# Optimization experiments

Hardware: AMD Instinct MI355X
Metric: run time of the kernel (lower is better)

The kernel has to match this reference:

```python
import jax, jax.numpy as jnp
import numpy as np

N_QUBITS = 10
DEPTH = 6


def _ry(theta):
    # RY(theta) = [[cos(t/2), -sin(t/2)], [sin(t/2), cos(t/2)]]
    c = jnp.cos(theta / 2)
    s = jnp.sin(theta / 2)
    return jnp.stack([jnp.stack([c, -s]), jnp.stack([s, c])]).astype(jnp.complex64)


def _rot(phi, theta, omega):
    # PennyLane Rot(phi, theta, omega) = RZ(omega) RY(theta) RZ(phi)
    c = jnp.cos(theta / 2)
    s = jnp.sin(theta / 2)
    ep = jnp.exp(-0.5j * (phi + omega).astype(jnp.complex64))
    em = jnp.exp(-0.5j * (phi - omega).astype(jnp.complex64))
    return jnp.stack([
        jnp.stack([ep * c, -jnp.conj(em) * s]),
        jnp.stack([em * s, jnp.conj(ep) * c]),
    ])


def _apply_1q(psi, U, w):
    # psi: (2,)*n statevector; apply 2x2 unitary U on qubit axis w
    psi = jnp.tensordot(U, psi, axes=([1], [w]))
    return jnp.moveaxis(psi, 0, w)


def _apply_cnot(psi, c, t):
    # flip target axis t on the control=1 slice of axis c
    psi = jnp.moveaxis(psi, (c, t), (0, 1))
    psi = jnp.concatenate([psi[:1], psi[1:, ::-1]], axis=0)
    return jnp.moveaxis(psi, (0, 1), (c, t))


def _circuit(angles, weights):
    """RY encoding + StronglyEntanglingLayers + PauliZ expvals. angles: (n,), weights: (depth, n, 3)."""
    n = N_QUBITS
    psi = jnp.zeros((2,) * n, jnp.complex64).at[(0,) * n].set(1.0)
    for i in range(n):
        psi = _apply_1q(psi, _ry(angles[i]), i)
    for l in range(DEPTH):
        for i in range(n):
            psi = _apply_1q(psi, _rot(weights[l, i, 0], weights[l, i, 1], weights[l, i, 2]), i)
        r = (l % (n - 1)) + 1  # default StronglyEntanglingLayers range schedule
        for i in range(n):
            psi = _apply_cnot(psi, i, (i + r) % n)
    p = psi.real ** 2 + psi.imag ** 2  # probabilities, shape (2,)*n
    exps = []
    for i in range(n):
        pm = jnp.moveaxis(p, i, 0).reshape(2, -1).sum(axis=1)
        exps.append(pm[0] - pm[1])  # <Z_i>
    return jnp.stack(exps)


def setup_inputs() -> dict:
    key = jax.random.key(0)
    ks = jax.random.split(key, 5)
    B, F, C = 8192, 1024, 10
    x = jax.random.normal(ks[0], (B, F), jnp.float32)
    W_proj = jax.random.normal(ks[1], (N_QUBITS, F), jnp.float32) / np.sqrt(F).astype(np.float32)
    weights = 0.01 * jax.random.normal(ks[2], (DEPTH, N_QUBITS, 3), jnp.float32)
    W_out = jax.random.normal(ks[3], (C, N_QUBITS), jnp.float32) / np.sqrt(N_QUBITS).astype(np.float32)
    b_out = 0.01 * jax.random.normal(ks[4], (C,), jnp.float32)
    return {"x": x, "W_proj": W_proj, "weights": weights, "W_out": W_out, "b_out": b_out}


def reference(x, W_proj, weights, W_out, b_out):
    # classical projection + angle encoding
    angles = jnp.tanh(x @ W_proj.T) * jnp.float32(np.pi / 2)  # (B, n_qubits)
    # batched exact statevector simulation of the VQC
    q = jax.vmap(_circuit, in_axes=(0, None))(angles, weights)  # (B, n_qubits)
    return q @ W_out.T + b_out  # (B, num_classes)
```

## Files before the change

kernel.cpp:

```cpp
#include <hip/hip_runtime.h>
#include <math.h>
#include <stdint.h>

#define NQ 10
#define DEPTH 6

typedef _Float16 f16x8 __attribute__((ext_vector_type(8)));
typedef float f32x4 __attribute__((ext_vector_type(4)));

typedef __attribute__((address_space(3))) unsigned int lds_u32;
typedef const __attribute__((address_space(1))) unsigned int glb_u32;

__device__ __forceinline__ void async_load16(const unsigned short* g, unsigned short* l) {
    __builtin_amdgcn_global_load_lds((glb_u32*)g, (lds_u32*)l, 16, 0, 0);
}

__device__ __forceinline__ void compute_gate(const float* __restrict__ weights,
                                             int idx, float* __restrict__ g) {
    float phi   = weights[idx * 3 + 0];
    float theta = weights[idx * 3 + 1];
    float omega = weights[idx * 3 + 2];
    float c = cosf(0.5f * theta), s = sinf(0.5f * theta);
    float ap = -0.5f * (phi + omega);
    float am = -0.5f * (phi - omega);
    float epr = cosf(ap), epi = sinf(ap);
    float emr = cosf(am), emi = sinf(am);
    g[0] =  epr * c;  g[1] =  epi * c;
    g[2] = -emr * s;  g[3] =  emi * s;
    g[4] =  emr * s;  g[5] =  emi * s;
    g[6] =  epr * c;  g[7] = -epi * c;
}

__global__ void prep_gates_kernel(const float* __restrict__ weights,
                                  float* __restrict__ gmat) {
    int idx = blockIdx.x * blockDim.x + threadIdx.x;
    if (idx >= DEPTH * NQ) return;
    compute_gate(weights, idx, gmat + idx * 8);
}

__device__ __forceinline__ void apply_1q_local(
    float (&ar)[16], float (&ai)[16], int q,
    float u00r, float u00i, float u01r, float u01i,
    float u10r, float u10i, float u11r, float u11i) {
#pragma unroll
    for (int j = 0; j < 16; ++j) {
        if ((j >> q) & 1) continue;
        int j1 = j | (1 << q);
        float a0r = ar[j],  a0i = ai[j];
        float a1r = ar[j1], a1i = ai[j1];
        ar[j]  = u00r*a0r - u00i*a0i + u01r*a1r - u01i*a1i;
        ai[j]  = u00r*a0i + u00i*a0r + u01r*a1i + u01i*a1r;
        ar[j1] = u10r*a0r - u10i*a0i + u11r*a1r - u11i*a1i;
        ai[j1] = u10r*a0i + u10i*a0r + u11r*a1i + u11i*a1r;
    }
}

__device__ __forceinline__ void apply_1q_lane(
    float (&ar)[16], float (&ai)[16], int q, int lane,
    float u00r, float u00i, float u01r, float u01i,
    float u10r, float u10i, float u11r, float u11i) {
    int  m  = 1 << (q - 4);
    bool hi = (lane >> (q - 4)) & 1;
    float car = hi ? u11r : u00r, cai = hi ? u11i : u00i;
    float cbr = hi ? u10r : u01r, cbi = hi ? u10i : u01i;
    float pr[16], pi[16];
#pragma unroll
    for (int j = 0; j < 16; ++j) pr[j] = __shfl_xor(ar[j], m, 64);
#pragma unroll
    for (int j = 0; j < 16; ++j) pi[j] = __shfl_xor(ai[j], m, 64);
#pragma unroll
    for (int j = 0; j < 16; ++j) {
        float mr = ar[j], mi = ai[j];
        ar[j] = car*mr - cai*mi + cbr*pr[j] - cbi*pi[j];
        ai[j] = car*mi + cai*mr + cbr*pi[j] + cbi*pr[j];
    }
}

__device__ __forceinline__ void cnot_gate(
    float (&ar)[16], float (&ai)[16], int c, int t, int lane) {
    if (c < 4 && t < 4) {
#pragma unroll
        for (int j = 0; j < 16; ++j) {
            if (((j >> c) & 1) && !((j >> t) & 1)) {
                int j1 = j | (1 << t);
                float tr = ar[j]; ar[j] = ar[j1]; ar[j1] = tr;
                float ti = ai[j]; ai[j] = ai[j1]; ai[j1] = ti;
            }
        }
    } else if (c < 4) {
        int m = 1 << (t - 4);
        float pr[16], pi[16];
#pragma unroll
        for (int j = 0; j < 16; ++j)
            if ((j >> c) & 1) pr[j] = __shfl_xor(ar[j], m, 64);
#pragma unroll
        for (int j = 0; j < 16; ++j)
            if ((j >> c) & 1) pi[j] = __shfl_xor(ai[j], m, 64);
#pragma unroll
        for (int j = 0; j < 16; ++j)
            if ((j >> c) & 1) { ar[j] = pr[j]; ai[j] = pi[j]; }
    } else if (t < 4) {
        bool cb = (lane >> (c - 4)) & 1;
#pragma unroll
        for (int j = 0; j < 16; ++j) {
            if (!((j >> t) & 1)) {
                int j1 = j | (1 << t);
                float lr = ar[j], li = ai[j], hr = ar[j1], hi2 = ai[j1];
                ar[j]  = cb ? hr : lr;  ai[j]  = cb ? hi2 : li;
                ar[j1] = cb ? lr : hr;  ai[j1] = cb ? li : hi2;
            }
        }
    } else {
        int  m  = 1 << (t - 4);
        bool cb = (lane >> (c - 4)) & 1;
        float pr[16], pi[16];
#pragma unroll
        for (int j = 0; j < 16; ++j) pr[j] = __shfl_xor(ar[j], m, 64);
#pragma unroll
        for (int j = 0; j < 16; ++j) pi[j] = __shfl_xor(ai[j], m, 64);
#pragma unroll
        for (int j = 0; j < 16; ++j) {
            ar[j] = cb ? pr[j] : ar[j];
            ai[j] = cb ? pi[j] : ai[j];
        }
    }
}

template <int R>
__device__ __forceinline__ void cnot_ring(float (&ar)[16], float (&ai)[16], int lane) {
#pragma unroll
    for (int i = 0; i < NQ; ++i) cnot_gate(ar, ai, i, (i + R) % NQ, lane);
}

template <int R>
__device__ __forceinline__ void cnot_ring_rev(float (&ar)[16], float (&ai)[16], int lane) {
#pragma unroll
    for (int i = NQ - 1; i >= 0; --i) cnot_gate(ar, ai, i, (i + R) % NQ, lane);
}

__device__ __forceinline__ void run_circuit(float (&ar)[16], float (&ai)[16],
                                            const float* __restrict__ gmat, int lane) {
    for (int l = 0; l < DEPTH; ++l) {
        const float* gl = gmat + l * (NQ * 8);
#pragma unroll
        for (int i = 0; i < NQ; ++i) {
            const float* g = gl + i * 8;
            float u00r = g[0], u00i = g[1], u01r = g[2], u01i = g[3];
            float u10r = g[4], u10i = g[5], u11r = g[6], u11i = g[7];
            if (i < 4)
                apply_1q_local(ar, ai, i, u00r,u00i,u01r,u01i,u10r,u10i,u11r,u11i);
            else
                apply_1q_lane(ar, ai, i, lane, u00r,u00i,u01r,u01i,u10r,u10i,u11r,u11i);
        }
        switch (l) {
            case 0: cnot_ring<1>(ar, ai, lane); break;
            case 1: cnot_ring<2>(ar, ai, lane); break;
            case 2: cnot_ring<3>(ar, ai, lane); break;
            case 3: cnot_ring<4>(ar, ai, lane); break;
            case 4: cnot_ring<5>(ar, ai, lane); break;
            default: cnot_ring<6>(ar, ai, lane); break;
        }
    }
}

__device__ __forceinline__ void run_circuit_T(float (&ar)[16], float (&ai)[16],
                                              const float* __restrict__ gmat, int lane) {
    for (int l = DEPTH - 1; l >= 0; --l) {
        switch (l) {
            case 0: cnot_ring_rev<1>(ar, ai, lane); break;
            case 1: cnot_ring_rev<2>(ar, ai, lane); break;
            case 2: cnot_ring_rev<3>(ar, ai, lane); break;
            case 3: cnot_ring_rev<4>(ar, ai, lane); break;
            case 4: cnot_ring_rev<5>(ar, ai, lane); break;
            default: cnot_ring_rev<6>(ar, ai, lane); break;
        }
        const float* gl = gmat + l * (NQ * 8);
#pragma unroll
        for (int i = 0; i < NQ; ++i) {
            const float* g = gl + i * 8;
            float u00r = g[0], u00i = g[1];
            float u01r = g[4], u01i = g[5];
            float u10r = g[2], u10i = g[3];
            float u11r = g[6], u11i = g[7];
            if (i < 4)
                apply_1q_local(ar, ai, i, u00r,u00i,u01r,u01i,u10r,u10i,u11r,u11i);
            else
                apply_1q_lane(ar, ai, i, lane, u00r,u00i,u01r,u01i,u10r,u10i,u11r,u11i);
        }
    }
}

__device__ __forceinline__ float wave_sum(float v) {
#pragma unroll
    for (int m = 1; m < 64; m <<= 1) v += __shfl_xor(v, m, 64);
    return v;
}

__device__ __forceinline__ void proj_v_body(
    const float* __restrict__ x, const float* __restrict__ Wproj,
    _Float16* __restrict__ V, int b, int lane) {
    const float4* xb4 = (const float4*)(x + (size_t)b * 1024);
    const float4* W4  = (const float4*)Wproj;
    float acc[NQ];
#pragma unroll
    for (int q = 0; q < NQ; ++q) acc[q] = 0.f;
#pragma unroll
    for (int k4 = 0; k4 < 4; ++k4) {
        float4 xv = xb4[k4 * 64 + lane];
#pragma unroll
        for (int q = 0; q < NQ; ++q) {
            float4 wv = W4[q * 256 + k4 * 64 + lane];
            acc[q] = fmaf(xv.x, wv.x, acc[q]);
            acc[q] = fmaf(xv.y, wv.y, acc[q]);
            acc[q] = fmaf(xv.z, wv.z, acc[q]);
            acc[q] = fmaf(xv.w, wv.w, acc[q]);
        }
    }
#pragma unroll
    for (int q = 0; q < NQ; ++q) acc[q] = wave_sum(acc[q]);

    float cq[NQ], sq[NQ];
#pragma unroll
    for (int q = 0; q < NQ; ++q) {
        float ang = tanhf(acc[q]) * 1.57079632679489662f;
        cq[q] = cosf(0.5f * ang);
        sq[q] = sinf(0.5f * ang);
    }
    float laneprod = 1.f;
#pragma unroll
    for (int q = 4; q < NQ; ++q)
        laneprod *= ((lane >> (q - 4)) & 1) ? sq[q] : cq[q];

    unsigned int buf[8];
#pragma unroll
    for (int jj = 0; jj < 8; ++jj) {
        unsigned short h2[2];
#pragma unroll
        for (int c = 0; c < 2; ++c) {
            int j = jj * 2 + c;
            float p = laneprod;
#pragma unroll
            for (int q = 0; q < 4; ++q) p *= ((j >> q) & 1) ? sq[q] : cq[q];
            h2[c] = __builtin_bit_cast(unsigned short, (_Float16)p);
        }
        buf[jj] = (unsigned int)h2[0] | ((unsigned int)h2[1] << 16);
    }
    uint4* dst = (uint4*)(V + (size_t)b * 1024 + 16 * lane);
    uint4 v0; v0.x = buf[0]; v0.y = buf[1]; v0.z = buf[2]; v0.w = buf[3];
    uint4 v1; v1.x = buf[4]; v1.y = buf[5]; v1.z = buf[6]; v1.w = buf[7];
    dst[0] = v0; dst[1] = v1;
}

__global__ __launch_bounds__(256) void basis_proj_kernel(
    const float* __restrict__ weights, _Float16* __restrict__ Bt,
    const float* __restrict__ x, const float* __restrict__ Wproj,
    _Float16* __restrict__ V, int B) {
    __shared__ float gmat_s[DEPTH * NQ * 8];
    int tid  = threadIdx.x;
    int lane = tid & 63;
    int w    = tid >> 6;

    if (blockIdx.x < 256) {
        if (tid < DEPTH * NQ) compute_gate(weights, tid, gmat_s + tid * 8);
        __syncthreads();

        int g = blockIdx.x * 4 + w;
        float ar[16], ai[16];
#pragma unroll
        for (int jj = 0; jj < 16; ++jj) {
            ar[jj] = (lane == (g >> 4) && jj == (g & 15)) ? 1.f : 0.f;
            ai[jj] = 0.f;
        }
        run_circuit_T(ar, ai, gmat_s, lane);

        unsigned int bufr[8], bufi[8];
#pragma unroll
        for (int jj = 0; jj < 8; ++jj) {
            unsigned short r0 = __builtin_bit_cast(unsigned short, (_Float16)ar[2*jj]);
            unsigned short r1 = __builtin_bit_cast(unsigned short, (_Float16)ar[2*jj+1]);
            unsigned short i0 = __builtin_bit_cast(unsigned short, (_Float16)ai[2*jj]);
            unsigned short i1 = __builtin_bit_cast(unsigned short, (_Float16)ai[2*jj+1]);
            bufr[jj] = (unsigned int)r0 | ((unsigned int)r1 << 16);
            bufi[jj] = (unsigned int)i0 | ((unsigned int)i1 << 16);
        }
        uint4* dre = (uint4*)((unsigned short*)Bt + (size_t)(2*g)     * 1024 + 16 * lane);
        uint4* dim = (uint4*)((unsigned short*)Bt + (size_t)(2*g + 1) * 1024 + 16 * lane);
        uint4 v;
        v.x = bufr[0]; v.y = bufr[1]; v.z = bufr[2]; v.w = bufr[3]; dre[0] = v;
        v.x = bufr[4]; v.y = bufr[5]; v.z = bufr[6]; v.w = bufr[7]; dre[1] = v;
        v.x = bufi[0]; v.y = bufi[1]; v.z = bufi[2]; v.w = bufi[3]; dim[0] = v;
        v.x = bufi[4]; v.y = bufi[5]; v.z = bufi[6]; v.w = bufi[7]; dim[1] = v;
    } else {
        int b = (blockIdx.x - 256) * 4 + w;
        if (b < B) proj_v_body(x, Wproj, V, b, lane);
    }
}

__global__ __launch_bounds__(256) void gemm_fused_kernel(
    const unsigned short* __restrict__ A,
    const unsigned short* __restrict__ Bt,
    float* __restrict__ Zpart) {
    __shared__ unsigned short As[128 * 64];
    __shared__ unsigned short Bs[128 * 64];
    int tid  = threadIdx.x;
    int lane = tid & 63;
    int w    = tid >> 6;
    int m0   = blockIdx.x * 128;
    int nb   = blockIdx.y;
    int n0   = nb * 128;
    int mh   = (w >> 1) * 64, nh = (w & 1) * 64;
    int quad = lane >> 4;
    int lrow = lane & 15;
    int srow  = (lane >> 3);
    int schnk = (lane & 7) ^ srow;

    f32x4 acc[4][4];
#pragma unroll
    for (int mi = 0; mi < 4; ++mi)
#pragma unroll
        for (int ni = 0; ni < 4; ++ni)
            acc[mi][ni] = (f32x4){0.f, 0.f, 0.f, 0.f};

    for (int kt = 0; kt < 16; ++kt) {
        if (kt) __syncthreads();
#pragma unroll
        for (int r = 0; r < 4; ++r) {
            int s   = w * 4 + r;
            int row = s * 8 + srow;
            async_load16(A  + (size_t)(m0 + row) * 1024 + kt * 64 + schnk * 8,
                         As + s * 512);
            async_load16(Bt + (size_t)(n0 + row) * 1024 + kt * 64 + schnk * 8,
                         Bs + s * 512);
        }
        asm volatile("s_waitcnt vmcnt(0)" ::: "memory");
        __syncthreads();
#pragma unroll
        for (int kk = 0; kk < 2; ++kk) {
            f16x8 af[4], bf[4];
#pragma unroll
            for (int i = 0; i < 4; ++i) {
                int cxa = (kk * 4 + quad) ^ (lrow & 7);
                af[i] = *(const f16x8*)(As + (mh + i * 16 + lrow) * 64 + cxa * 8);
                bf[i] = *(const f16x8*)(Bs + (nh + i * 16 + lrow) * 64 + cxa * 8);
            }
#pragma unroll
            for (int mi = 0; mi < 4; ++mi)
#pragma unroll
                for (int ni = 0; ni < 4; ++ni)
                    acc[mi][ni] = __builtin_amdgcn_mfma_f32_16x16x32_f16(
                        af[mi], bf[ni], acc[mi][ni], 0, 0, 0);
        }
    }

    __syncthreads();
    float* Zs = (float*)As;
#pragma unroll
    for (int mi = 0; mi < 4; ++mi) {
#pragma unroll
        for (int r = 0; r < 4; ++r) {
            float p0 = acc[mi][0][r] * acc[mi][0][r];
            float p1 = acc[mi][1][r] * acc[mi][1][r];
            float p2 = acc[mi][2][r] * acc[mi][2][r];
            float p3 = acc[mi][3][r] * acc[mi][3][r];
            float t0 = (p0 + p1) + (p2 + p3);
            float t3 = (p0 - p1) + (p2 - p3);
            float t4 = (p0 + p1) - (p2 + p3);
            t0 += __shfl_xor(t0, 1, 64);
            t3 += __shfl_xor(t3, 1, 64);
            t4 += __shfl_xor(t4, 1, 64);
            float u2 = __shfl_xor(t0, 2, 64);
            float ap = t0 + u2;
            float am = (lane & 2) ? u2 - t0 : t0 - u2;
            t3 += __shfl_xor(t3, 2, 64);
            t4 += __shfl_xor(t4, 2, 64);
            float u4  = __shfl_xor(ap, 4, 64);
            float bpp = ap + u4;
            float bpm = (lane & 4) ? u4 - ap : ap - u4;
            float bmp = am + __shfl_xor(am, 4, 64);
            t3 += __shfl_xor(t3, 4, 64);
            t4 += __shfl_xor(t4, 4, 64);
            float u8 = __shfl_xor(bpp, 8, 64);
            float T  = bpp + u8;
            float Z2 = (lane & 8) ? u8 - bpp : bpp - u8;
            float Z1 = bpm + __shfl_xor(bpm, 8, 64);
            float Z0 = bmp + __shfl_xor(bmp, 8, 64);
            t3 += __shfl_xor(t3, 8, 64);
            t4 += __shfl_xor(t4, 8, 64);
            if (lrow == 0) {
                int row = mh + mi * 16 + quad * 4 + r;
                float* z = Zs + ((size_t)(w & 1) * 128 + row) * 9;
                z[0] = T;  z[1] = Z0; z[2] = Z1; z[3] = Z2;
                z[4] = t3; z[5] = t4;
            }
        }
    }
    __syncthreads();
    {
        int row  = tid >> 1, part = tid & 1;
        const float* za = Zs + (size_t)row * 9;
        const float* zb = Zs + (size_t)(128 + row) * 9;
        float o[4];
        if (part == 0) {
            o[0] = za[0] + zb[0];
            o[1] = za[1] + zb[1];
            o[2] = za[2] + zb[2];
            o[3] = za[3] + zb[3];
        } else {
            o[0] = za[4] + zb[4];
            o[1] = za[5] + zb[5];
            o[2] = za[0] - zb[0];
            o[3] = 0.f;
        }
        float4 v = {o[0], o[1], o[2], o[3]};
        *(float4*)(Zpart + ((size_t)(m0 + row) * 16 + nb) * 8 + part * 4) = v;
    }
}

__global__ __launch_bounds__(256) void combine_head_kernel(
    const float* __restrict__ Zpart, const float* __restrict__ Wout,
    const float* __restrict__ bout, float* __restrict__ out, int B) {
    int lane = threadIdx.x & 63;
    int wid  = threadIdx.x >> 6;
    int b    = blockIdx.x * 4 + wid;
    if (b >= B) return;

    float z[8];
    if (lane < 16) {
        const float4* p = (const float4*)(Zpart + ((size_t)b * 16 + lane) * 8);
        float4 a = p[0], c = p[1];
        z[0]=a.x; z[1]=a.y; z[2]=a.z; z[3]=a.w; z[4]=c.x; z[5]=c.y; z[6]=c.z; z[7]=c.w;
    } else {
#pragma unroll
        for (int i = 0; i < 8; ++i) z[i] = 0.f;
    }
    float Zq[NQ];
#pragma unroll
    for (int q = 0; q < 6; ++q) {
        float v = z[q + 1];
        v += __shfl_xor(v, 1, 64);
        v += __shfl_xor(v, 2, 64);
        v += __shfl_xor(v, 4, 64);
        v += __shfl_xor(v, 8, 64);
        Zq[q] = v;
    }
    {
        float T = z[0];
        float u1 = __shfl_xor(T, 1, 64);
        float P  = T + u1;
        float M  = (lane & 1) ? u1 - T : T - u1;
        float u2 = __shfl_xor(P, 2, 64);
        float PP = P + u2;
        float PM = (lane & 2) ? u2 - P : P - u2;
        float MP = M + __shfl_xor(M, 2, 64);
        float u4  = __shfl_xor(PP, 4, 64);
        float PPP = PP + u4;
        float PPM = (lane & 4) ? u4 - PP : PP - u4;
        float PMP = PM + __shfl_xor(PM, 4, 64);
        float MPP = MP + __shfl_xor(MP, 4, 64);
        float u8 = __shfl_xor(PPP, 8, 64);
        Zq[9] = (lane & 8) ? u8 - PPP : PPP - u8;
        Zq[8] = PPM + __shfl_xor(PPM, 8, 64);
        Zq[7] = PMP + __shfl_xor(PMP, 8, 64);
        Zq[6] = MPP + __shfl_xor(MPP, 8, 64);
    }
    if (lane < NQ) {
        float o = bout[lane];
#pragma unroll
        for (int q = 0; q < NQ; ++q) o = fmaf(Zq[q], Wout[lane * NQ + q], o);
        out[(size_t)b * NQ + lane] = o;
    }
}

__global__ __launch_bounds__(256) void vqc_kernel(
    const float* __restrict__ x, const float* __restrict__ Wproj,
    const float* __restrict__ gmat, const float* __restrict__ Wout,
    const float* __restrict__ bout, float* __restrict__ out, int B) {
    int lane = threadIdx.x & 63;
    int wid  = threadIdx.x >> 6;
    int b    = blockIdx.x * 4 + wid;
    if (b >= B) return;

    const float* xb = x + (size_t)b * 1024;
    float acc[NQ];
#pragma unroll
    for (int q = 0; q < NQ; ++q) acc[q] = 0.f;
#pragma unroll
    for (int k = 0; k < 16; ++k) {
        float xv = xb[k * 64 + lane];
#pragma unroll
        for (int q = 0; q < NQ; ++q)
            acc[q] = fmaf(xv, Wproj[q * 1024 + k * 64 + lane], acc[q]);
    }
#pragma unroll
    for (int q = 0; q < NQ; ++q) acc[q] = wave_sum(acc[q]);

    float cq[NQ], sq[NQ];
#pragma unroll
    for (int q = 0; q < NQ; ++q) {
        float ang = tanhf(acc[q]) * 1.57079632679489662f;
        cq[q] = cosf(0.5f * ang);
        sq[q] = sinf(0.5f * ang);
    }
    float laneprod = 1.f;
#pragma unroll
    for (int q = 4; q < NQ; ++q)
        laneprod *= ((lane >> (q - 4)) & 1) ? sq[q] : cq[q];
    float ar[16], ai[16];
#pragma unroll
    for (int j = 0; j < 16; ++j) {
        float p = laneprod;
#pragma unroll
        for (int q = 0; q < 4; ++q) p *= ((j >> q) & 1) ? sq[q] : cq[q];
        ar[j] = p; ai[j] = 0.f;
    }
    run_circuit(ar, ai, gmat, lane);

    float T = 0.f, S[4] = {0.f, 0.f, 0.f, 0.f};
#pragma unroll
    for (int j = 0; j < 16; ++j) {
        float p = ar[j] * ar[j] + ai[j] * ai[j];
        T += p;
#pragma unroll
        for (int q = 0; q < 4; ++q) S[q] += ((j >> q) & 1) ? -p : p;
    }
    float Zq[NQ];
#pragma unroll
    for (int q = 0; q < 4; ++q) Zq[q] = S[q];
#pragma unroll
    for (int q = 4; q < NQ; ++q) Zq[q] = ((lane >> (q - 4)) & 1) ? -T : T;
#pragma unroll
    for (int q = 0; q < NQ; ++q) Zq[q] = wave_sum(Zq[q]);
    if (lane < NQ) {
        float o = bout[lane];
#pragma unroll
        for (int q = 0; q < NQ; ++q) o = fmaf(Zq[q], Wout[lane * NQ + q], o);
        out[(size_t)b * NQ + lane] = o;
    }
}

extern "C" void kernel_launch(void* const* d_in, const int* in_sizes, int n_in,
                              void* d_out, int out_size, void* d_ws, size_t ws_size,
                              hipStream_t stream) {
    const float* x       = (const float*)d_in[0];
    const float* Wproj   = (const float*)d_in[1];
    const float* weights = (const float*)d_in[2];
    const float* Wout    = (const float*)d_in[3];
    const float* bout    = (const float*)d_in[4];
    float* out = (float*)d_out;
    int B = in_sizes[0] / 1024;

    char* ws = (char*)d_ws;
    size_t off_Bt = 4096;
    size_t off_V  = off_Bt + (size_t)2048 * 1024 * 2;
    size_t off_Z  = off_V  + (size_t)B * 1024 * 2;
    size_t need   = off_Z  + (size_t)B * 16 * 8 * 4;

    if (ws_size >= need && (B % 128) == 0) {
        _Float16* Bt = (_Float16*)(ws + off_Bt);
        _Float16* V  = (_Float16*)(ws + off_V);
        float*  Zprt = (float*)(ws + off_Z);

        basis_proj_kernel<<<256 + B / 4, 256, 0, stream>>>(weights, Bt, x, Wproj, V, B);
        gemm_fused_kernel<<<dim3(B / 128, 16), 256, 0, stream>>>(
            (const unsigned short*)V, (const unsigned short*)Bt, Zprt);
        combine_head_kernel<<<B / 4, 256, 0, stream>>>(Zprt, Wout, bout, out, B);
    } else {
        float* gmat = (float*)ws;
        prep_gates_kernel<<<1, 64, 0, stream>>>(weights, gmat);
        vqc_kernel<<<(B + 3) / 4, 256, 0, stream>>>(x, Wproj, gmat, Wout, bout, out, B);
    }
}
```

Measured before the change: 163.0 us.

## Enlarge GEMM tile to 256x256 with double-buffered async LDS prefetch

The fused GEMM kernel moves from 128x128 tiles with 4 waves to 256x256 tiles with 8 waves. It double-buffers the LDS K-slices, prefetching the next slice with async global-to-LDS loads while MFMAs run on the current one, and raises wave priority around the MFMA block. The epilogue now reduces two 128-column N sub-blocks per workgroup. The aim is to hide global load latency and raise operand reuse per LDS byte. The cost is 128KB of LDS and 128 accumulator registers per thread, which limits each CU to one block. The grid also shrinks to 256 workgroups, which may leave load imbalance or lower occupancy.

```diff
diff --git a/kernel.cpp b/kernel.cpp
--- a/kernel.cpp
+++ b/kernel.cpp
@@ -296,66 +296,88 @@
     }
 }
 
-__global__ __launch_bounds__(256) void gemm_fused_kernel(
+#define STAGE(buf, kt_) do {                                                        \
+    unsigned short* As_ = lds_s + (buf) * 32768;                                    \
+    unsigned short* Bs_ = As_ + 16384;                                              \
+    _Pragma("unroll")                                                               \
+    for (int r_ = 0; r_ < 4; ++r_) {                                                \
+        int s_   = w * 4 + r_;                                                      \
+        int row_ = s_ * 8 + srow;                                                   \
+        async_load16(A  + (size_t)(m0 + row_) * 1024 + (kt_) * 64 + schnk * 8,      \
+                     As_ + s_ * 512);                                               \
+        async_load16(Bt + (size_t)(n0 + row_) * 1024 + (kt_) * 64 + schnk * 8,      \
+                     Bs_ + s_ * 512);                                               \
+    }                                                                               \
+} while (0)
+
+__global__ __launch_bounds__(512, 2) void gemm_fused_kernel(
     const unsigned short* __restrict__ A,
     const unsigned short* __restrict__ Bt,
     float* __restrict__ Zpart) {
-    __shared__ unsigned short As[128 * 64];
-    __shared__ unsigned short Bs[128 * 64];
+    __shared__ __align__(16) unsigned short lds_s[2 * 32768];
     int tid  = threadIdx.x;
     int lane = tid & 63;
     int w    = tid >> 6;
-    int m0   = blockIdx.x * 128;
-    int nb   = blockIdx.y;
-    int n0   = nb * 128;
-    int mh   = (w >> 1) * 64, nh = (w & 1) * 64;
+    int wm   = w >> 2;
+    int wn   = w & 3;
+    int by   = blockIdx.x & 7;
+    int bx   = blockIdx.x >> 3;
+    int m0   = bx * 256;
+    int n0   = by * 256;
     int quad = lane >> 4;
     int lrow = lane & 15;
     int srow  = (lane >> 3);
     int schnk = (lane & 7) ^ srow;
 
-    f32x4 acc[4][4];
-#pragma unroll
-    for (int mi = 0; mi < 4; ++mi)
+    f32x4 acc[8][4];
+#pragma unroll
+    for (int mi = 0; mi < 8; ++mi)
 #pragma unroll
         for (int ni = 0; ni < 4; ++ni)
             acc[mi][ni] = (f32x4){0.f, 0.f, 0.f, 0.f};
 
+    STAGE(0, 0);
+
+#pragma unroll 2
     for (int kt = 0; kt < 16; ++kt) {
-        if (kt) __syncthreads();
-#pragma unroll
-        for (int r = 0; r < 4; ++r) {
-            int s   = w * 4 + r;
-            int row = s * 8 + srow;
-            async_load16(A  + (size_t)(m0 + row) * 1024 + kt * 64 + schnk * 8,
-                         As + s * 512);
-            async_load16(Bt + (size_t)(n0 + row) * 1024 + kt * 64 + schnk * 8,
-                         Bs + s * 512);
-        }
-        asm volatile("s_waitcnt vmcnt(0)" ::: "memory");
-        __syncthreads();
+        int cur = kt & 1;
+        if (kt < 15) {
+            STAGE(cur ^ 1, kt + 1);
+            asm volatile("s_waitcnt vmcnt(8)" ::: "memory");
+        } else {
+            asm volatile("s_waitcnt vmcnt(0)" ::: "memory");
+        }
+        __builtin_amdgcn_s_barrier();
+        asm volatile("" ::: "memory");
+        const unsigned short* As_ = lds_s + cur * 32768;
+        const unsigned short* Bs_ = As_ + 16384;
 #pragma unroll
         for (int kk = 0; kk < 2; ++kk) {
-            f16x8 af[4], bf[4];
-#pragma unroll
-            for (int i = 0; i < 4; ++i) {
-                int cxa = (kk * 4 + quad) ^ (lrow & 7);
-                af[i] = *(const f16x8*)(As + (mh + i * 16 + lrow) * 64 + cxa * 8);
-                bf[i] = *(const f16x8*)(Bs + (nh + i * 16 + lrow) * 64 + cxa * 8);
-            }
-#pragma unroll
-            for (int mi = 0; mi < 4; ++mi)
+            int cx = (kk * 4 + quad) ^ (lrow & 7);
+            f16x8 bf[4];
+#pragma unroll
+            for (int ni = 0; ni < 4; ++ni)
+                bf[ni] = *(const f16x8*)(Bs_ + (wn * 64 + ni * 16 + lrow) * 64 + cx * 8);
+            __builtin_amdgcn_s_setprio(1);
+#pragma unroll
+            for (int mi = 0; mi < 8; ++mi) {
+                f16x8 af = *(const f16x8*)(As_ + (wm * 128 + mi * 16 + lrow) * 64 + cx * 8);
 #pragma unroll
                 for (int ni = 0; ni < 4; ++ni)
                     acc[mi][ni] = __builtin_amdgcn_mfma_f32_16x16x32_f16(
-                        af[mi], bf[ni], acc[mi][ni], 0, 0, 0);
-        }
-    }
-
-    __syncthreads();
-    float* Zs = (float*)As;
-#pragma unroll
-    for (int mi = 0; mi < 4; ++mi) {
+                        af, bf[ni], acc[mi][ni], 0, 0, 0);
+            }
+            __builtin_amdgcn_s_setprio(0);
+        }
+        asm volatile("" ::: "memory");
+        __builtin_amdgcn_s_barrier();
+    }
+
+    float* Zs = (float*)lds_s;
+    int nbl  = wn >> 1;
+    int half = wn & 1;
+#pragma unroll
+    for (int mi = 0; mi < 8; ++mi) {
 #pragma unroll
         for (int r = 0; r < 4; ++r) {
             float p0 = acc[mi][0][r] * acc[mi][0][r];
@@ -387,8 +409,8 @@
             t3 += __shfl_xor(t3, 8, 64);
             t4 += __shfl_xor(t4, 8, 64);
             if (lrow == 0) {
-                int row = mh + mi * 16 + quad * 4 + r;
-                float* z = Zs + ((size_t)(w & 1) * 128 + row) * 9;
+                int row = wm * 128 + mi * 16 + quad * 4 + r;
+                float* z = Zs + ((size_t)(nbl * 2 + half) * 256 + row) * 9;
                 z[0] = T;  z[1] = Z0; z[2] = Z1; z[3] = Z2;
                 z[4] = t3; z[5] = t4;
             }
@@ -397,22 +419,25 @@
     __syncthreads();
     {
         int row  = tid >> 1, part = tid & 1;
-        const float* za = Zs + (size_t)row * 9;
-        const float* zb = Zs + (size_t)(128 + row) * 9;
-        float o[4];
-        if (part == 0) {
-            o[0] = za[0] + zb[0];
-            o[1] = za[1] + zb[1];
-            o[2] = za[2] + zb[2];
-            o[3] = za[3] + zb[3];
-        } else {
-            o[0] = za[4] + zb[4];
-            o[1] = za[5] + zb[5];
-            o[2] = za[0] - zb[0];
-            o[3] = 0.f;
-        }
-        float4 v = {o[0], o[1], o[2], o[3]};
-        *(float4*)(Zpart + ((size_t)(m0 + row) * 16 + nb) * 8 + part * 4) = v;
+#pragma unroll
+        for (int nb = 0; nb < 2; ++nb) {
+            const float* za = Zs + ((size_t)(nb * 2 + 0) * 256 + row) * 9;
+            const float* zb = Zs + ((size_t)(nb * 2 + 1) * 256 + row) * 9;
+            float o[4];
+            if (part == 0) {
+                o[0] = za[0] + zb[0];
+                o[1] = za[1] + zb[1];
+                o[2] = za[2] + zb[2];
+                o[3] = za[3] + zb[3];
+            } else {
+                o[0] = za[4] + zb[4];
+                o[1] = za[5] + zb[5];
+                o[2] = za[0] - zb[0];
+                o[3] = 0.f;
+            }
+            float4 v = {o[0], o[1], o[2], o[3]};
+            *(float4*)(Zpart + ((size_t)(m0 + row) * 16 + (by * 2 + nb)) * 8 + part * 4) = v;
+        }
     }
 }
 
@@ -555,13 +580,13 @@
     size_t off_Z  = off_V  + (size_t)B * 1024 * 2;
     size_t need   = off_Z  + (size_t)B * 16 * 8 * 4;
 
-    if (ws_size >= need && (B % 128) == 0) {
+    if (ws_size >= need && (B % 256) == 0) {
         _Float16* Bt = (_Float16*)(ws + off_Bt);
         _Float16* V  = (_Float16*)(ws + off_V);
         float*  Zprt = (float*)(ws + off_Z);
 
         basis_proj_kernel<<<256 + B / 4, 256, 0, stream>>>(weights, Bt, x, Wproj, V, B);
-        gemm_fused_kernel<<<dim3(B / 128, 16), 256, 0, stream>>>(
+        gemm_fused_kernel<<<(B / 256) * 8, 512, 0, stream>>>(
             (const unsigned short*)V, (const unsigned short*)Bt, Zprt);
         combine_head_kernel<<<B / 4, 256, 0, stream>>>(Zprt, Wout, bout, out, B);
     } else {
```

New measurement: 160.7 us. Within noise of the previous version (-1.4%).
